# Kernel tuning notes

Hardware: AMD Instinct MI355X
Metric: run time of the kernel (lower is better)

## Reference

```python
import jax, jax.numpy as jnp
import numpy as np

K = 8          # num groups
SIZE = 250     # state/hidden size (h1 = h2 = 250)
M = 576        # flattened input size (24x24)
B = 2048       # batch
HA = 100       # attention hidden
EPS = 1e-5


def _ln(x, g, b):
    mu = jnp.mean(x, axis=-1, keepdims=True)
    v = jnp.mean(jnp.square(x - mu), axis=-1, keepdims=True)
    return (x - mu) * jax.lax.rsqrt(v + EPS) * g + b


def setup_inputs() -> dict:
    key = jax.random.key(0)
    ks = jax.random.split(key, 10)
    def w(k, shape):
        return jax.random.normal(k, shape, jnp.float32) / np.sqrt(shape[0]).astype(np.float32)
    inp = {
        "x": jax.random.normal(ks[0], (B * K, M), jnp.float32),
        "state": jax.random.normal(ks[1], (B * K, SIZE), jnp.float32),
        # encoder: Linear(SIZE,250) + ReLU + LN(250)
        "enc_W": w(ks[2], (SIZE, 250)), "enc_b": jnp.zeros((250,), jnp.float32),
        "enc_g": jnp.ones((250,), jnp.float32), "enc_bt": jnp.zeros((250,), jnp.float32),
        # core: Linear(500,250) + ReLU + LN(250)
        "core_W": w(ks[3], (500, 250)), "core_b": jnp.zeros((250,), jnp.float32),
        "core_g": jnp.ones((250,), jnp.float32), "core_bt": jnp.zeros((250,), jnp.float32),
        # context: Linear(250,250) + ReLU + LN(250)
        "ctx_W": w(ks[4], (250, 250)), "ctx_b": jnp.zeros((250,), jnp.float32),
        "ctx_g": jnp.ones((250,), jnp.float32), "ctx_bt": jnp.zeros((250,), jnp.float32),
        # attention: Linear(250,100)+Tanh+LN(100)+Linear(100,1)+Sigmoid
        "att_W1": w(ks[5], (250, HA)), "att_b1": jnp.zeros((HA,), jnp.float32),
        "att_g": jnp.ones((HA,), jnp.float32), "att_bt": jnp.zeros((HA,), jnp.float32),
        "att_W2": w(ks[6], (HA, 1)), "att_b2": jnp.zeros((1,), jnp.float32),
        # output: Linear(250 + 250 + M, SIZE)
        "out_W": w(ks[7], (250 + 250 + M, SIZE)), "out_b": jnp.zeros((SIZE,), jnp.float32),
    }
    return inp


def reference(x, state, enc_W, enc_b, enc_g, enc_bt, core_W, core_b, core_g, core_bt,
              ctx_W, ctx_b, ctx_g, ctx_bt, att_W1, att_b1, att_g, att_bt,
              att_W2, att_b2, out_W, out_b):
    bk = state.shape[0]
    b = bk // K
    h1 = 250
    # 0-1. encode state -> [B*K, h1]
    s1 = _ln(jax.nn.relu(state @ enc_W + enc_b), enc_g, enc_bt)
    s1r = s1.reshape(b, K, h1)
    # 2-3. focus / context pairs via static gather index [K, K-1]
    idx = np.array([[j for j in range(K) if j != i] for i in range(K)], np.int32)
    cs = s1r[:, idx]                                    # [b, K, K-1, h1]
    fs = jnp.broadcast_to(s1r[:, :, None, :], cs.shape)  # [b, K, K-1, h1]
    # 4. concat pairs -> [b*K*(K-1), 2*h1]
    concat = jnp.concatenate([fs, cs], axis=-1).reshape(b * K * (K - 1), 2 * h1)
    # 5. core MLP
    core_out = _ln(jax.nn.relu(concat @ core_W + core_b), core_g, core_bt)
    # context MLP
    context_out = _ln(jax.nn.relu(core_out @ ctx_W + ctx_b), ctx_g, ctx_bt)
    # attention scalar per pair
    att_h = _ln(jnp.tanh(core_out @ att_W1 + att_b1), att_g, att_bt)
    att = jax.nn.sigmoid(att_h @ att_W2 + att_b2)        # [b*K*(K-1), 1]
    # 6-7. attention-weighted sum over K-1 context effects -> [B*K, h2]
    effect_sum = jnp.sum(context_out.reshape(bk, K - 1, h1) * att.reshape(bk, K - 1, 1), axis=1)
    # 8. decode
    total = jnp.concatenate([s1, effect_sum, x], axis=1)  # [B*K, h1+h2+M]
    new_state = total @ out_W + out_b                     # [B*K, SIZE]
    return new_state
```

## Files before the change

### kernel.cpp

```cpp
#include <hip/hip_runtime.h>
#include <math.h>

#define KK 8
#define H 250
#define MDIM 576
#define NB 2048
#define HA 100
#define ROWS (NB*KK)
#define PROWS (ROWS*7)
#define PQS 512
#define KP 1088
#define EPS 1e-5f

typedef unsigned short ushort_t;
typedef short short8 __attribute__((ext_vector_type(8)));
typedef unsigned short us8 __attribute__((ext_vector_type(8)));
typedef unsigned short us4 __attribute__((ext_vector_type(4)));
typedef unsigned short us2 __attribute__((ext_vector_type(2)));
typedef float f32x4 __attribute__((ext_vector_type(4)));

template<int CTRL>
__device__ __forceinline__ float dpp_add_f32(float x) {
    const int s = __builtin_amdgcn_update_dpp(
        0, __builtin_bit_cast(int, x), CTRL, 0xF, 0xF, true);
    return x + __builtin_bit_cast(float, s);
}
__device__ __forceinline__ float wave_sum_dpp(float x) {
    x = dpp_add_f32<0x111>(x);
    x = dpp_add_f32<0x112>(x);
    x = dpp_add_f32<0x114>(x);
    x = dpp_add_f32<0x118>(x);
    x = dpp_add_f32<0x142>(x);
    x = dpp_add_f32<0x143>(x);
    return __builtin_bit_cast(float, __builtin_amdgcn_readlane(
        __builtin_bit_cast(int, x), 63));
}
__device__ __forceinline__ float bfly16_sum(float x) {
    x = dpp_add_f32<0xB1>(x);
    x = dpp_add_f32<0x4E>(x);
    x = dpp_add_f32<0x141>(x);
    x = dpp_add_f32<0x140>(x);
    return x;
}

__device__ __forceinline__ void async_copy16(const void* g, void* l) {
    __builtin_amdgcn_global_load_lds(
        (const __attribute__((address_space(1))) void*)g,
        (__attribute__((address_space(3))) void*)l, 16, 0, 0);
}

__device__ __forceinline__ ushort_t f2bf(float v) {
    union { float f; unsigned int u; } c; c.f = v;
    unsigned int x = c.u;
    x += 0x7fff + ((x >> 16) & 1);
    return (ushort_t)(x >> 16);
}
__device__ __forceinline__ float bf2f(ushort_t v) {
    union { unsigned int u; float f; } c; c.u = ((unsigned int)v) << 16;
    return c.f;
}
__device__ __forceinline__ float ftanh(float x) {
    const float e = __expf(2.f * x);
    return 1.f - 2.f * __builtin_amdgcn_rcpf(e + 1.f);
}
__device__ __forceinline__ float fsigmoid(float x) {
    return __builtin_amdgcn_rcpf(1.f + __expf(-x));
}

__global__ __launch_bounds__(256) void k_prep(
    const float* __restrict__ out_W, const float* __restrict__ core_W,
    const float* __restrict__ ctx_W, const float* __restrict__ att_W1,
    const float* __restrict__ enc_W, const float* __restrict__ state,
    const float* __restrict__ x,
    ushort_t* __restrict__ Wt, ushort_t* __restrict__ Wpq,
    ushort_t* __restrict__ Wca, ushort_t* __restrict__ Wenc,
    ushort_t* __restrict__ Sb, ushort_t* __restrict__ Abuf)
{
    const int b = blockIdx.x, t = threadIdx.x;
    if (b < 256) {
        const int n = b;
        for (int k = t; k < KP; k += 256) {
            const float v = (n < H && k < 1076) ? out_W[(size_t)k * H + n] : 0.f;
            Wt[(size_t)n * KP + k] = f2bf(v);
        }
    } else if (b < 768) {
        const int n = b - 256, k = t;
        float v = 0.f;
        if (k < H) {
            if (n < H)                    v = core_W[(size_t)k * H + n];
            else if (n >= 256 && n < 506) v = core_W[(size_t)(H + k) * H + (n - 256)];
        }
        Wpq[(size_t)n * 256 + k] = f2bf(v);
    } else if (b < 1152) {
        const int n = b - 768, k = t;
        float v = 0.f;
        if (k < H) {
            if (n < H)           v = ctx_W[(size_t)k * H + n];
            else if (n < H + HA) v = att_W1[(size_t)k * HA + (n - H)];
        }
        Wca[(size_t)n * 256 + k] = f2bf(v);
    } else if (b < 1408) {
        const int n = b - 1152, k = t;
        const float v = (n < H && k < H) ? enc_W[(size_t)k * H + n] : 0.f;
        Wenc[(size_t)n * 256 + k] = f2bf(v);
    } else if (b < 2432) {
        const int r0 = (b - 1408) * 16;
        for (int idx = t; idx < 16 * 256; idx += 256) {
            const int r = r0 + (idx >> 8), k = idx & 255;
            const float v = (k < H) ? state[(size_t)r * H + k] : 0.f;
            Sb[(size_t)r * 256 + k] = f2bf(v);
        }
    } else {
        const int r0 = (b - 2432) * 16;
        for (int idx = t; idx < 16 * 588; idx += 256) {
            const int r = r0 + idx / 588, c = 500 + idx % 588;
            const float v = (c < 500 + MDIM) ? x[(size_t)r * MDIM + (c - 500)] : 0.f;
            Abuf[(size_t)r * KP + c] = f2bf(v);
        }
    }
}

template<int NT>
__global__ __launch_bounds__(512, NT == 8 ? 2 : 4) void k_gemm_nres(
    const ushort_t* __restrict__ A, int lda,
    const ushort_t* __restrict__ B, int ldb,
    void* __restrict__ Cp, int ldc,
    const float* __restrict__ bias,
    int ksteps, int nlim, int bf16out)
{
    constexpr int NROWS = NT * 64;
    __shared__ __align__(16) ushort_t As[64 * 32];
    __shared__ __align__(16) ushort_t Bs[NROWS * 32];
    const int tid = threadIdx.x, lane = tid & 63, wave = tid >> 6;
    const int wm = wave >> 2, wn = wave & 3;
    const int R0 = (int)blockIdx.x * 64;

    const int ar = tid >> 2, acb = tid & 3;
    const bool aon = tid < 256;
    const int acl = acb ^ ((ar >> 1) & 3);
    const ushort_t* gA = A + (size_t)(R0 + ar) * lda + acl * 8;

    const int q = lane >> 4, fr = lane & 15;

    f32x4 acc[2][NT] = {};
    for (int ks = 0; ks < ksteps; ++ks) {
        const int k0 = ks * 32;
        if (aon) async_copy16(gA + k0, &As[tid * 8]);
#pragma unroll
        for (int it = 0; it < NT / 2; ++it) {
            const int ci  = it * 512 + tid;
            const int rb  = ci >> 2, cb2 = ci & 3;
            const int clb = cb2 ^ ((rb >> 1) & 3);
            async_copy16(B + (size_t)rb * ldb + k0 + clb * 8, &Bs[ci * 8]);
        }
        __syncthreads();
        short8 a[2];
#pragma unroll
        for (int ms = 0; ms < 2; ++ms) {
            const int row = wm * 32 + ms * 16 + fr;
            a[ms] = *(const short8*)&As[(row * 4 + (q ^ ((row >> 1) & 3))) * 8];
        }
#pragma unroll
        for (int nt = 0; nt < NT; ++nt) {
            const int n = wn * (NT * 16) + nt * 16 + fr;
            const short8 b = *(const short8*)&Bs[(n * 4 + (q ^ ((n >> 1) & 3))) * 8];
#pragma unroll
            for (int ms = 0; ms < 2; ++ms)
                acc[ms][nt] = __builtin_amdgcn_mfma_f32_16x16x32_bf16(
                    a[ms], b, acc[ms][nt], 0, 0, 0);
        }
        __syncthreads();
    }

#pragma unroll
    for (int ms = 0; ms < 2; ++ms)
#pragma unroll
        for (int nt = 0; nt < NT; ++nt) {
            const int col = wn * (NT * 16) + nt * 16 + fr;
            if (col >= nlim) continue;
            const float bv = bias ? bias[col] : 0.f;
#pragma unroll
            for (int reg = 0; reg < 4; ++reg) {
                const int row = R0 + wm * 32 + ms * 16 + q * 4 + reg;
                const float v = acc[ms][nt][reg] + bv;
                if (bf16out) ((ushort_t*)Cp)[(size_t)row * ldc + col] = f2bf(v);
                else         ((float*)Cp)[(size_t)row * ldc + col] = v;
            }
        }
}

__global__ __launch_bounds__(256) void k_lnenc(const ushort_t* __restrict__ Epre,
    const float* __restrict__ eb, const float* __restrict__ eg,
    const float* __restrict__ ebt, ushort_t* __restrict__ Abuf)
{
    const int wave = threadIdx.x >> 6, lane = threadIdx.x & 63;
    const int row = blockIdx.x * 4 + wave;
    const int c0 = 4 * lane;

    const us4 v = *(const us4*)&Epre[(size_t)row * 256 + c0];
    float y[4]; float sm = 0.f, sq = 0.f;
#pragma unroll
    for (int t = 0; t < 4; ++t) {
        const int cc = c0 + t;
        float z = 0.f;
        if (cc < H) z = fmaxf(bf2f(v[t]) + eb[cc], 0.f);
        y[t] = z; sm += z; sq += z * z;
    }
    sm = wave_sum_dpp(sm);
    sq = wave_sum_dpp(sq);
    const float mu = sm * (1.f / H);
    const float rs = __builtin_amdgcn_rsqf(sq * (1.f / H) - mu * mu + EPS);
    ushort_t o[4];
#pragma unroll
    for (int t = 0; t < 4; ++t) {
        const int cc = c0 + t;
        o[t] = (cc < H) ? f2bf((y[t] - mu) * rs * eg[cc] + ebt[cc]) : (ushort_t)0;
    }
    ushort_t* dst = Abuf + (size_t)row * KP + c0;
    if (c0 + 3 < H) { *(us4*)dst = (us4){o[0], o[1], o[2], o[3]}; }
    else {
        if (c0 + 1 < H) *(us2*)dst = (us2){o[0], o[1]};
    }
}

__global__ __launch_bounds__(256) void k_core(const ushort_t* __restrict__ PQb,
    const float* __restrict__ core_b, const float* __restrict__ core_g,
    const float* __restrict__ core_bt, ushort_t* __restrict__ Co)
{
    const int wave = threadIdx.x >> 6, lane = threadIdx.x & 63;
    const int g = blockIdx.x * 4 + wave;
    const int i = g & 7;
    const int c = lane * 4;

    const us4 pu = *(const us4*)&PQb[(size_t)g * PQS + c];
    us4 qu[7];
#pragma unroll
    for (int jj = 0; jj < 7; ++jj) {
        const int j = jj + (jj >= i ? 1 : 0);
        const int qr = (g & ~7) + j;
        qu[jj] = *(const us4*)&PQb[(size_t)qr * PQS + 256 + c];
    }
    float pe[4], cb[4], cg[4], cbt[4]; bool vl[4];
#pragma unroll
    for (int t = 0; t < 4; ++t) {
        vl[t]  = (c + t) < H;
        pe[t]  = bf2f(pu[t]);
        cb[t]  = vl[t] ? core_b[c + t]  : 0.f;
        cg[t]  = vl[t] ? core_g[c + t]  : 0.f;
        cbt[t] = vl[t] ? core_bt[c + t] : 0.f;
    }
    float z[7][4], red[7][2];
#pragma unroll
    for (int jj = 0; jj < 7; ++jj) {
        float sm = 0.f, sq = 0.f;
#pragma unroll
        for (int t = 0; t < 4; ++t) {
            const float zz = vl[t] ? fmaxf(pe[t] + bf2f(qu[jj][t]) + cb[t], 0.f) : 0.f;
            z[jj][t] = zz; sm += zz; sq = fmaf(zz, zz, sq);
        }
        red[jj][0] = sm; red[jj][1] = sq;
    }
#pragma unroll
    for (int jj = 0; jj < 7; ++jj) {
        red[jj][0] = wave_sum_dpp(red[jj][0]);
        red[jj][1] = wave_sum_dpp(red[jj][1]);
    }
#pragma unroll
    for (int jj = 0; jj < 7; ++jj) {
        const float mu = red[jj][0] * (1.f / H);
        const float rs = __builtin_amdgcn_rsqf(red[jj][1] * (1.f / H) - mu * mu + EPS);
        us4 o;
#pragma unroll
        for (int t = 0; t < 4; ++t)
            o[t] = vl[t] ? f2bf((z[jj][t] - mu) * rs * cg[t] + cbt[t]) : (ushort_t)0;
        *(us4*)&Co[((size_t)g * 7 + jj) * 256 + c] = o;
    }
}

__global__ __launch_bounds__(512, 4) void k_cs(
    const ushort_t* __restrict__ Co,
    const ushort_t* __restrict__ Wca,
    const float* __restrict__ ctx_b,
    const float* __restrict__ att_b1, const float* __restrict__ att_g,
    const float* __restrict__ attW2,
    ushort_t* __restrict__ Cs, float* __restrict__ Srow)
{
    __shared__ __align__(16) ushort_t As[64 * 32];
    __shared__ __align__(16) ushort_t Bs[384 * 32];
    const int tid = threadIdx.x, lane = tid & 63, wave = tid >> 6;
    const int wm = wave >> 1, wn = wave & 1;
    (void)wm; (void)wn;
    const int wmm = wave >> 2, wnn = wave & 3;
    const int R0 = (int)blockIdx.x * 64;

    const int ar = tid >> 2, acb = tid & 3;
    const bool aon = tid < 256;
    const int acl = acb ^ ((ar >> 1) & 3);
    const ushort_t* gA = Co + (size_t)(R0 + ar) * 256 + acl * 8;

    const int q = lane >> 4, fr = lane & 15;

    f32x4 acc[2][6] = {};
    for (int ks = 0; ks < 8; ++ks) {
        const int k0 = ks * 32;
        if (aon) async_copy16(gA + k0, &As[tid * 8]);
#pragma unroll
        for (int it = 0; it < 3; ++it) {
            const int ci  = it * 512 + tid;
            const int rb  = ci >> 2, cb2 = ci & 3;
            const int clb = cb2 ^ ((rb >> 1) & 3);
            async_copy16(Wca + (size_t)rb * 256 + k0 + clb * 8, &Bs[ci * 8]);
        }
        __syncthreads();
        short8 a[2];
#pragma unroll
        for (int ms = 0; ms < 2; ++ms) {
            const int row = wmm * 32 + ms * 16 + fr;
            a[ms] = *(const short8*)&As[(row * 4 + (q ^ ((row >> 1) & 3))) * 8];
        }
#pragma unroll
        for (int nt = 0; nt < 6; ++nt) {
            const int n = wnn * 96 + nt * 16 + fr;
            const short8 b = *(const short8*)&Bs[(n * 4 + (q ^ ((n >> 1) & 3))) * 8];
#pragma unroll
            for (int ms = 0; ms < 2; ++ms)
                acc[ms][nt] = __builtin_amdgcn_mfma_f32_16x16x32_bf16(
                    a[ms], b, acc[ms][nt], 0, 0, 0);
        }
        __syncthreads();
    }

    bool eC[6], eA[6]; float b_[6], gw[6];
#pragma unroll
    for (int nt = 0; nt < 6; ++nt) {
        const int col = wnn * 96 + nt * 16 + fr;
        eC[nt] = col < H;
        eA[nt] = (col >= H) && (col < H + HA);
        if (eC[nt])      { b_[nt] = ctx_b[col];      gw[nt] = 0.f; }
        else if (eA[nt]) { const int ca = col - H;
                           b_[nt] = att_b1[ca];
                           gw[nt] = att_g[ca] * attW2[ca]; }
        else             { b_[nt] = gw[nt] = 0.f; }
    }

#pragma unroll
    for (int ms = 0; ms < 2; ++ms) {
        float smc[4] = {}, sqc[4] = {}, sma[4] = {}, sqa[4] = {}, szgw[4] = {};
#pragma unroll
        for (int nt = 0; nt < 6; ++nt) {
#pragma unroll
            for (int reg = 0; reg < 4; ++reg) {
                const float val = acc[ms][nt][reg] + b_[nt];
                if (eC[nt]) {
                    const float zz = fmaxf(val, 0.f);
                    acc[ms][nt][reg] = zz;
                    smc[reg] += zz; sqc[reg] = fmaf(zz, zz, sqc[reg]);
                } else if (eA[nt]) {
                    const float za = ftanh(val);
                    sma[reg] += za; sqa[reg] = fmaf(za, za, sqa[reg]);
                    szgw[reg] = fmaf(za, gw[nt], szgw[reg]);
                }
            }
        }
#pragma unroll
        for (int reg = 0; reg < 4; ++reg) {
            smc[reg]  = bfly16_sum(smc[reg]);
            sqc[reg]  = bfly16_sum(sqc[reg]);
            sma[reg]  = bfly16_sum(sma[reg]);
            sqa[reg]  = bfly16_sum(sqa[reg]);
            szgw[reg] = bfly16_sum(szgw[reg]);
        }
        if (fr == 0) {
#pragma unroll
            for (int reg = 0; reg < 4; ++reg) {
                const int row = R0 + wmm * 32 + ms * 16 + q * 4 + reg;
                *(f32x4*)&Srow[(size_t)row * 32 + wnn * 8] =
                    (f32x4){smc[reg], sqc[reg], sma[reg], sqa[reg]};
                Srow[(size_t)row * 32 + wnn * 8 + 4] = szgw[reg];
            }
        }
#pragma unroll
        for (int nt = 0; nt < 6; ++nt) {
            const int col = wnn * 96 + nt * 16 + fr;
            if (col >= 256) continue;
#pragma unroll
            for (int reg = 0; reg < 4; ++reg) {
                const int row = R0 + wmm * 32 + ms * 16 + q * 4 + reg;
                Cs[(size_t)row * 256 + col] =
                    eC[nt] ? f2bf(acc[ms][nt][reg]) : (ushort_t)0;
            }
        }
    }
}

__global__ __launch_bounds__(256) void k_eff2(
    const ushort_t* __restrict__ Cs, const float* __restrict__ Srow,
    const float* __restrict__ ctx_g, const float* __restrict__ ctx_bt,
    const float* __restrict__ att_g, const float* __restrict__ att_bt,
    const float* __restrict__ attW2, const float* __restrict__ att_b2,
    ushort_t* __restrict__ Abuf)
{
    const int wave = threadIdx.x >> 6, lane = threadIdx.x & 63;
    const int g = blockIdx.x * 4 + wave;
    const int c0 = 4 * lane;

    float psg = 0.f, psb = 0.f;
    for (int c = lane; c < HA; c += 64) {
        const float w2 = attW2[c];
        psg = fmaf(att_g[c], w2, psg);
        psb = fmaf(att_bt[c], w2, psb);
    }
    psg = wave_sum_dpp(psg); psb = wave_sum_dpp(psb);
    const float sgw = psg;
    const float ab2 = att_b2[0] + psb;

    float g4[4], bt4[4];
#pragma unroll
    for (int t = 0; t < 4; ++t) {
        const bool vl = (c0 + t) < H;
        g4[t]  = vl ? ctx_g[c0 + t]  : 0.f;
        bt4[t] = vl ? ctx_bt[c0 + t] : 0.f;
    }

    us4 zv[7];
#pragma unroll
    for (int jj = 0; jj < 7; ++jj)
        zv[jj] = *(const us4*)&Cs[((size_t)g * 7 + jj) * 256 + c0];

    float A4[4] = {0.f, 0.f, 0.f, 0.f};
    float S0 = 0.f, S1 = 0.f;
#pragma unroll
    for (int jj = 0; jj < 7; ++jj) {
        const float* sr = Srow + ((size_t)g * 7 + jj) * 32;
        float s0 = 0.f, s1 = 0.f, s2 = 0.f, s3 = 0.f, s4 = 0.f;
#pragma unroll
        for (int w = 0; w < 4; ++w) {
            const f32x4 v = *(const f32x4*)&sr[w * 8];
            s0 += v[0]; s1 += v[1]; s2 += v[2]; s3 += v[3];
            s4 += sr[w * 8 + 4];
        }
        const float muC = s0 * (1.f / H);
        const float rsC = __builtin_amdgcn_rsqf(s1 * (1.f / H) - muC * muC + EPS);
        const float muA = s2 * (1.f / HA);
        const float rsA = __builtin_amdgcn_rsqf(s3 * (1.f / HA) - muA * muA + EPS);
        const float dot = rsA * (s4 - muA * sgw) + ab2;
        const float ag  = fsigmoid(dot);
        const float cj  = ag * rsC;
        S0 += ag; S1 = fmaf(cj, muC, S1);
#pragma unroll
        for (int e = 0; e < 4; ++e)
            A4[e] = fmaf(cj, bf2f(zv[jj][e]), A4[e]);
    }
    ushort_t o[4];
#pragma unroll
    for (int e = 0; e < 4; ++e)
        o[e] = f2bf(g4[e] * (A4[e] - S1) + bt4[e] * S0);
    ushort_t* dst = Abuf + (size_t)g * KP + H + c0;
    if (c0 + 1 < H) *(us2*)dst       = (us2){o[0], o[1]};
    if (c0 + 3 < H) *(us2*)(dst + 2) = (us2){o[2], o[3]};
}

extern "C" void kernel_launch(void* const* d_in, const int* in_sizes, int n_in,
                              void* d_out, int out_size, void* d_ws, size_t ws_size,
                              hipStream_t stream)
{
    const float* x      = (const float*)d_in[0];
    const float* state  = (const float*)d_in[1];
    const float* enc_W  = (const float*)d_in[2];
    const float* enc_b  = (const float*)d_in[3];
    const float* enc_g  = (const float*)d_in[4];
    const float* enc_bt = (const float*)d_in[5];
    const float* core_W = (const float*)d_in[6];
    const float* core_b = (const float*)d_in[7];
    const float* core_g = (const float*)d_in[8];
    const float* core_bt= (const float*)d_in[9];
    const float* ctx_W  = (const float*)d_in[10];
    const float* ctx_b  = (const float*)d_in[11];
    const float* ctx_g  = (const float*)d_in[12];
    const float* ctx_bt = (const float*)d_in[13];
    const float* att_W1 = (const float*)d_in[14];
    const float* att_b1 = (const float*)d_in[15];
    const float* att_g  = (const float*)d_in[16];
    const float* att_bt = (const float*)d_in[17];
    const float* att_W2 = (const float*)d_in[18];
    const float* att_b2 = (const float*)d_in[19];
    const float* out_W  = (const float*)d_in[20];
    const float* out_b  = (const float*)d_in[21];
    float* out = (float*)d_out;

    ushort_t* Abuf = (ushort_t*)d_ws;
    ushort_t* Wt   = Abuf + (size_t)ROWS * KP;
    ushort_t* Wpq  = Wt + (size_t)256 * KP;
    ushort_t* Wca  = Wpq + (size_t)512 * 256;
    ushort_t* Wenc = Wca + (size_t)384 * 256;
    ushort_t* Co   = Wenc + (size_t)256 * 256;
    ushort_t* Cs   = Co + (size_t)PROWS * 256;
    float*    Srow = (float*)(Cs + (size_t)PROWS * 256);
    ushort_t* Sb   = Cs;
    ushort_t* Epre = Sb + (size_t)ROWS * 256;
    ushort_t* PQb  = Epre + (size_t)ROWS * 256;

    k_prep  <<<3456, 256, 0, stream>>>(out_W, core_W, ctx_W, att_W1, enc_W,
                                       state, x, Wt, Wpq, Wca, Wenc, Sb, Abuf);
    k_gemm_nres<4><<<ROWS / 64, 512, 0, stream>>>(Sb, 256, Wenc, 256, Epre, 256,
                                                  nullptr, 8, 256, 1);
    k_lnenc <<<ROWS / 4, 256, 0, stream>>>(Epre, enc_b, enc_g, enc_bt, Abuf);
    k_gemm_nres<8><<<ROWS / 64, 512, 0, stream>>>(Abuf, KP, Wpq, 256, PQb, PQS,
                                                  nullptr, 8, 512, 1);
    k_core  <<<ROWS / 4, 256, 0, stream>>>(PQb, core_b, core_g, core_bt, Co);
    k_cs    <<<PROWS / 64, 512, 0, stream>>>(Co, Wca, ctx_b, att_b1, att_g,
                                             att_W2, Cs, Srow);
    k_eff2  <<<ROWS / 4, 256, 0, stream>>>(Cs, Srow, ctx_g, ctx_bt,
                                           att_g, att_bt, att_W2, att_b2, Abuf);
    k_gemm_nres<4><<<ROWS / 64, 512, 0, stream>>>(Abuf, KP, Wt, KP, out, H,
                                                  out_b, KP / 32, 250, 0);
}
```

Baseline: 339.8 us.

## Double-buffer LDS tiles in GEMM and context/attention kernels to overlap loads

```diff
diff --git a/kernel.cpp b/kernel.cpp
--- a/kernel.cpp
+++ b/kernel.cpp
@@ -128,9 +128,12 @@
     const float* __restrict__ bias,
     int ksteps, int nlim, int bf16out)
 {
+    constexpr bool DB = (NT <= 4);
     constexpr int NROWS = NT * 64;
-    __shared__ __align__(16) ushort_t As[64 * 32];
-    __shared__ __align__(16) ushort_t Bs[NROWS * 32];
+    constexpr int ASZ = 64 * 32;
+    constexpr int BSZ = NROWS * 32;
+    __shared__ __align__(16) ushort_t As[(DB ? 2 : 1) * ASZ];
+    __shared__ __align__(16) ushort_t Bs[(DB ? 2 : 1) * BSZ];
     const int tid = threadIdx.x, lane = tid & 63, wave = tid >> 6;
     const int wm = wave >> 2, wn = wave & 3;
     const int R0 = (int)blockIdx.x * 64;
@@ -143,33 +146,74 @@
     const int q = lane >> 4, fr = lane & 15;
 
     f32x4 acc[2][NT] = {};
-    for (int ks = 0; ks < ksteps; ++ks) {
-        const int k0 = ks * 32;
-        if (aon) async_copy16(gA + k0, &As[tid * 8]);
-#pragma unroll
-        for (int it = 0; it < NT / 2; ++it) {
-            const int ci  = it * 512 + tid;
-            const int rb  = ci >> 2, cb2 = ci & 3;
-            const int clb = cb2 ^ ((rb >> 1) & 3);
-            async_copy16(B + (size_t)rb * ldb + k0 + clb * 8, &Bs[ci * 8]);
-        }
+
+    if constexpr (DB) {
+        auto stage = [&](int ks, int p) {
+            const int k0 = ks * 32;
+            if (aon) async_copy16(gA + k0, &As[p * ASZ + tid * 8]);
+#pragma unroll
+            for (int it = 0; it < NT / 2; ++it) {
+                const int ci  = it * 512 + tid;
+                const int rb  = ci >> 2, cb2 = ci & 3;
+                const int clb = cb2 ^ ((rb >> 1) & 3);
+                async_copy16(B + (size_t)rb * ldb + k0 + clb * 8,
+                             &Bs[p * BSZ + ci * 8]);
+            }
+        };
+        stage(0, 0);
         __syncthreads();
-        short8 a[2];
-#pragma unroll
-        for (int ms = 0; ms < 2; ++ms) {
-            const int row = wm * 32 + ms * 16 + fr;
-            a[ms] = *(const short8*)&As[(row * 4 + (q ^ ((row >> 1) & 3))) * 8];
-        }
-#pragma unroll
-        for (int nt = 0; nt < NT; ++nt) {
-            const int n = wn * (NT * 16) + nt * 16 + fr;
-            const short8 b = *(const short8*)&Bs[(n * 4 + (q ^ ((n >> 1) & 3))) * 8];
-#pragma unroll
-            for (int ms = 0; ms < 2; ++ms)
-                acc[ms][nt] = __builtin_amdgcn_mfma_f32_16x16x32_bf16(
-                    a[ms], b, acc[ms][nt], 0, 0, 0);
-        }
-        __syncthreads();
+        int p = 0;
+        for (int ks = 0; ks < ksteps; ++ks) {
+            if (ks + 1 < ksteps) stage(ks + 1, p ^ 1);
+            short8 a[2];
+#pragma unroll
+            for (int ms = 0; ms < 2; ++ms) {
+                const int row = wm * 32 + ms * 16 + fr;
+                a[ms] = *(const short8*)&As[p * ASZ +
+                        (row * 4 + (q ^ ((row >> 1) & 3))) * 8];
+            }
+#pragma unroll
+            for (int nt = 0; nt < NT; ++nt) {
+                const int n = wn * (NT * 16) + nt * 16 + fr;
+                const short8 b = *(const short8*)&Bs[p * BSZ +
+                        (n * 4 + (q ^ ((n >> 1) & 3))) * 8];
+#pragma unroll
+                for (int ms = 0; ms < 2; ++ms)
+                    acc[ms][nt] = __builtin_amdgcn_mfma_f32_16x16x32_bf16(
+                        a[ms], b, acc[ms][nt], 0, 0, 0);
+            }
+            __syncthreads();
+            p ^= 1;
+        }
+    } else {
+        for (int ks = 0; ks < ksteps; ++ks) {
+            const int k0 = ks * 32;
+            if (aon) async_copy16(gA + k0, &As[tid * 8]);
+#pragma unroll
+            for (int it = 0; it < NT / 2; ++it) {
+                const int ci  = it * 512 + tid;
+                const int rb  = ci >> 2, cb2 = ci & 3;
+                const int clb = cb2 ^ ((rb >> 1) & 3);
+                async_copy16(B + (size_t)rb * ldb + k0 + clb * 8, &Bs[ci * 8]);
+            }
+            __syncthreads();
+            short8 a[2];
+#pragma unroll
+            for (int ms = 0; ms < 2; ++ms) {
+                const int row = wm * 32 + ms * 16 + fr;
+                a[ms] = *(const short8*)&As[(row * 4 + (q ^ ((row >> 1) & 3))) * 8];
+            }
+#pragma unroll
+            for (int nt = 0; nt < NT; ++nt) {
+                const int n = wn * (NT * 16) + nt * 16 + fr;
+                const short8 b = *(const short8*)&Bs[(n * 4 + (q ^ ((n >> 1) & 3))) * 8];
+#pragma unroll
+                for (int ms = 0; ms < 2; ++ms)
+                    acc[ms][nt] = __builtin_amdgcn_mfma_f32_16x16x32_bf16(
+                        a[ms], b, acc[ms][nt], 0, 0, 0);
+            }
+            __syncthreads();
+        }
     }
 
 #pragma unroll
@@ -285,11 +329,11 @@
     const float* __restrict__ attW2,
     ushort_t* __restrict__ Cs, float* __restrict__ Srow)
 {
-    __shared__ __align__(16) ushort_t As[64 * 32];
-    __shared__ __align__(16) ushort_t Bs[384 * 32];
+    constexpr int ASZ = 64 * 32;
+    constexpr int BSZ = 384 * 32;
+    __shared__ __align__(16) ushort_t As[2 * ASZ];
+    __shared__ __align__(16) ushort_t Bs[2 * BSZ];
     const int tid = threadIdx.x, lane = tid & 63, wave = tid >> 6;
-    const int wm = wave >> 1, wn = wave & 1;
-    (void)wm; (void)wn;
     const int wmm = wave >> 2, wnn = wave & 3;
     const int R0 = (int)blockIdx.x * 64;
 
@@ -300,34 +344,44 @@
 
     const int q = lane >> 4, fr = lane & 15;
 
-    f32x4 acc[2][6] = {};
-    for (int ks = 0; ks < 8; ++ks) {
+    auto stage = [&](int ks, int p) {
         const int k0 = ks * 32;
-        if (aon) async_copy16(gA + k0, &As[tid * 8]);
+        if (aon) async_copy16(gA + k0, &As[p * ASZ + tid * 8]);
 #pragma unroll
         for (int it = 0; it < 3; ++it) {
             const int ci  = it * 512 + tid;
             const int rb  = ci >> 2, cb2 = ci & 3;
             const int clb = cb2 ^ ((rb >> 1) & 3);
-            async_copy16(Wca + (size_t)rb * 256 + k0 + clb * 8, &Bs[ci * 8]);
-        }
-        __syncthreads();
+            async_copy16(Wca + (size_t)rb * 256 + k0 + clb * 8,
+                         &Bs[p * BSZ + ci * 8]);
+        }
+    };
+
+    f32x4 acc[2][6] = {};
+    stage(0, 0);
+    __syncthreads();
+    int p = 0;
+    for (int ks = 0; ks < 8; ++ks) {
+        if (ks + 1 < 8) stage(ks + 1, p ^ 1);
         short8 a[2];
 #pragma unroll
         for (int ms = 0; ms < 2; ++ms) {
             const int row = wmm * 32 + ms * 16 + fr;
-            a[ms] = *(const short8*)&As[(row * 4 + (q ^ ((row >> 1) & 3))) * 8];
+            a[ms] = *(const short8*)&As[p * ASZ +
+                    (row * 4 + (q ^ ((row >> 1) & 3))) * 8];
         }
 #pragma unroll
         for (int nt = 0; nt < 6; ++nt) {
             const int n = wnn * 96 + nt * 16 + fr;
-            const short8 b = *(const short8*)&Bs[(n * 4 + (q ^ ((n >> 1) & 3))) * 8];
+            const short8 b = *(const short8*)&Bs[p * BSZ +
+                    (n * 4 + (q ^ ((n >> 1) & 3))) * 8];
 #pragma unroll
             for (int ms = 0; ms < 2; ++ms)
                 acc[ms][nt] = __builtin_amdgcn_mfma_f32_16x16x32_bf16(
                     a[ms], b, acc[ms][nt], 0, 0, 0);
         }
         __syncthreads();
+        p ^= 1;
     }
 
     bool eC[6], eA[6]; float b_[6], gw[6];
```

After: 337.4 us. No clear change (-0.7%).
